# Kernel optimization log

Measured on AMD Instinct MI355X. Metric: run time of the kernel, lower is better.

The kernel has to match this reference:

```python
import jax, jax.numpy as jnp
import numpy as np

FILTERS = 256
B, H, W = 16, 64, 64
LN_EPS = 1e-5


def setup_inputs() -> dict:
    key = jax.random.key(0)
    ks = jax.random.split(key, 6)
    C = FILTERS
    scale = 1.0 / np.sqrt(C)  # kaiming-ish init for 1x1 convs
    return {
        "x": jax.random.normal(ks[0], (B, C, H, W), dtype=jnp.float32),
        "g": jax.random.normal(ks[1], (B, C, H, W), dtype=jnp.float32),
        "Wx": jax.random.normal(ks[2], (C, C), dtype=jnp.float32) * scale,
        "Wg": jax.random.normal(ks[3], (C, C), dtype=jnp.float32) * scale,
        "Wpsi": jax.random.normal(ks[4], (1, C), dtype=jnp.float32) * scale,
        "ln_gamma": jnp.ones((C,), dtype=jnp.float32),
        "ln_beta": jnp.zeros((C,), dtype=jnp.float32),
        "bxg": jnp.zeros((C,), dtype=jnp.float32),
        "bpsi": jnp.zeros((1,), dtype=jnp.float32),
    }


def reference(x, g, Wx, Wg, Wpsi, ln_gamma, ln_beta, bxg, bpsi):
    # 1x1 convs == per-pixel channel GEMMs: [B,C,H,W] x [O,C] -> [B,O,H,W]
    x_conv = jnp.einsum("bchw,oc->bohw", x, Wx)
    g_conv = jnp.einsum("bchw,oc->bohw", g, Wg)
    att = jax.nn.relu(x_conv + g_conv + bxg[None, :, None, None])
    # LayerNorm over channel dim (original permutes to NHWC, LN over last dim)
    mean = jnp.mean(att, axis=1, keepdims=True)
    var = jnp.mean(jnp.square(att - mean), axis=1, keepdims=True)
    att = (att - mean) * jax.lax.rsqrt(var + LN_EPS)
    att = att * ln_gamma[None, :, None, None] + ln_beta[None, :, None, None]
    # psi: 1x1 conv to single channel + bias, sigmoid gate
    att = jnp.einsum("bchw,oc->bohw", att, Wpsi) + bpsi[None, :, None, None]
    att = jax.nn.sigmoid(att)  # [B,1,H,W]
    return att * x
```

## Files before the change

kernel.cpp:

```cpp
#include <hip/hip_runtime.h>
#include <stdint.h>


typedef __bf16 bf16x8 __attribute__((ext_vector_type(8)));
typedef float f32x4 __attribute__((ext_vector_type(4)));

#define STR 40
#define LN_EPS 1e-5f

__device__ __forceinline__ uint16_t f2b(float f) {
    union { float f; uint32_t i; } v; v.f = f;
    uint32_t x = v.i;
    return (uint16_t)((x + 0x7FFFu + ((x >> 16) & 1u)) >> 16);
}

struct EpiShared {
    float red[3][4][256];
    float psi[256];
    float cpart[8];
};

union ALds {
    uint16_t a[2][2][256 * STR];
    EpiShared e;
};

__global__ void wconv_kernel(const float* __restrict__ Wx, const float* __restrict__ Wg,
                             uint16_t* __restrict__ ox, uint16_t* __restrict__ og) {
    const int i  = blockIdx.x * 256 + threadIdx.x;
    const int n  = i >> 6;
    const int k4 = (i & 63) * 4;
    const int it = k4 >> 5;
    const int kk = k4 & 31;
    const int dst = it * 8192 + n * 32 + kk;
    const float4 a = *(const float4*)&Wx[n * 256 + k4];
    const float4 b = *(const float4*)&Wg[n * 256 + k4];
    uint2 pa, pb;
    pa.x = (uint32_t)f2b(a.x) | ((uint32_t)f2b(a.y) << 16);
    pa.y = (uint32_t)f2b(a.z) | ((uint32_t)f2b(a.w) << 16);
    pb.x = (uint32_t)f2b(b.x) | ((uint32_t)f2b(b.y) << 16);
    pb.y = (uint32_t)f2b(b.z) | ((uint32_t)f2b(b.w) << 16);
    *(uint2*)&ox[dst] = pa;
    *(uint2*)&og[dst] = pb;
}

__device__ __forceinline__ void stage_load(float av[16], const float* __restrict__ Asrc,
                                           size_t abase, int c0, int px) {
    #pragma unroll
    for (int j = 0; j < 2; ++j)
        #pragma unroll
        for (int c = 0; c < 8; ++c)
            av[j * 8 + c] = Asrc[abase + (size_t)(c0 + j * 16 + c) * 4096 + px];
}

__device__ __forceinline__ void stage_store(const float av[16], uint16_t* dstrow, int c0) {
    #pragma unroll
    for (int j = 0; j < 2; ++j) {
        uint4 w;
        w.x = (uint32_t)f2b(av[j*8+0]) | ((uint32_t)f2b(av[j*8+1]) << 16);
        w.y = (uint32_t)f2b(av[j*8+2]) | ((uint32_t)f2b(av[j*8+3]) << 16);
        w.z = (uint32_t)f2b(av[j*8+4]) | ((uint32_t)f2b(av[j*8+5]) << 16);
        w.w = (uint32_t)f2b(av[j*8+6]) | ((uint32_t)f2b(av[j*8+7]) << 16);
        *(uint4*)&dstrow[c0 + j * 16] = w;
    }
}

__global__ __launch_bounds__(1024) void attgate_kernel(
    const float* __restrict__ x,
    const float* __restrict__ g,
    const uint16_t* __restrict__ Wxb,
    const uint16_t* __restrict__ Wgb,
    const float* __restrict__ Wpsi,
    const float* __restrict__ gamma,
    const float* __restrict__ beta,
    const float* __restrict__ bxg,
    const float* __restrict__ bpsi,
    float* __restrict__ out)
{
    __shared__ __align__(16) ALds u;

    const int t    = threadIdx.x;
    const int lane = t & 63;
    const int wv   = t >> 6;
    const int os   = wv & 3;
    const int ps   = wv >> 2;
    const int ln   = lane & 15;
    const int q    = lane >> 4;

    const int gp0  = blockIdx.x * 256;
    const int b    = gp0 >> 12;
    const int pix0 = gp0 & 4095;
    const size_t xbase = (size_t)b * (256 * 4096) + pix0;

    f32x4 acc[4][4];
    #pragma unroll
    for (int i = 0; i < 4; ++i)
        #pragma unroll
        for (int j = 0; j < 4; ++j)
            acc[i][j] = (f32x4){0.f, 0.f, 0.f, 0.f};

    const int at  = t & 511;
    const int px  = at & 255;
    const int cg  = at >> 8;
    const int c0  = cg * 8;
    const float* Asrc = (t < 512) ? x : g;
    const int tens    = (t < 512) ? 0 : 1;

    float av[16];
    stage_load(av, Asrc, xbase, c0, px);
    stage_store(av, &u.a[0][tens][px * STR], c0);

    const int fro = os * 64 + ln;

    for (int it = 0; it < 8; ++it) {
        __syncthreads();
        const int cur = it & 1;
        const uint16_t* Wxi = Wxb + it * 8192;
        const uint16_t* Wgi = Wgb + it * 8192;

        bf16x8 bx[4];
        #pragma unroll
        for (int nt = 0; nt < 4; ++nt)
            bx[nt] = *(const bf16x8*)&Wxi[(fro + nt * 16) * 32 + q * 8];

        if (it < 7)
            stage_load(av, Asrc, xbase + (size_t)((it + 1) * 32) * 4096, c0, px);

        bf16x8 af[4];
        #pragma unroll
        for (int mt = 0; mt < 4; ++mt)
            af[mt] = *(const bf16x8*)&u.a[cur][0][(ps * 64 + mt * 16 + ln) * STR + q * 8];
        #pragma unroll
        for (int mt = 0; mt < 4; ++mt)
            #pragma unroll
            for (int nt = 0; nt < 4; ++nt)
                acc[mt][nt] = __builtin_amdgcn_mfma_f32_16x16x32_bf16(af[mt], bx[nt], acc[mt][nt], 0, 0, 0);

        bf16x8 bg[4];
        #pragma unroll
        for (int nt = 0; nt < 4; ++nt)
            bg[nt] = *(const bf16x8*)&Wgi[(fro + nt * 16) * 32 + q * 8];
        #pragma unroll
        for (int mt = 0; mt < 4; ++mt)
            af[mt] = *(const bf16x8*)&u.a[cur][1][(ps * 64 + mt * 16 + ln) * STR + q * 8];
        #pragma unroll
        for (int mt = 0; mt < 4; ++mt)
            #pragma unroll
            for (int nt = 0; nt < 4; ++nt)
                acc[mt][nt] = __builtin_amdgcn_mfma_f32_16x16x32_bf16(af[mt], bg[nt], acc[mt][nt], 0, 0, 0);

        if (it < 7)
            stage_store(av, &u.a[cur ^ 1][tens][px * STR], c0);
    }

    __syncthreads();

    if (t < 256) {
        float a  = Wpsi[t] * gamma[t];
        float bb = Wpsi[t] * beta[t];
        #pragma unroll
        for (int off = 32; off; off >>= 1) {
            a  += __shfl_xor(a, off, 64);
            bb += __shfl_xor(bb, off, 64);
        }
        if (lane == 0) { u.e.cpart[wv] = a; u.e.cpart[4 + wv] = bb; }
    }

    float biasv[4], Ac[4];
    #pragma unroll
    for (int nt = 0; nt < 4; ++nt) {
        const int o = os * 64 + nt * 16 + ln;
        biasv[nt] = bxg[o];
        Ac[nt]    = Wpsi[o] * gamma[o];
    }
    __syncthreads();
    const float sumA = u.e.cpart[0] + u.e.cpart[1] + u.e.cpart[2] + u.e.cpart[3];
    const float sumB = u.e.cpart[4] + u.e.cpart[5] + u.e.cpart[6] + u.e.cpart[7];

    #pragma unroll
    for (int mt = 0; mt < 4; ++mt) {
        #pragma unroll
        for (int r = 0; r < 4; ++r) {
            float s = 0.f, ss = 0.f, tt = 0.f;
            #pragma unroll
            for (int nt = 0; nt < 4; ++nt) {
                float v = acc[mt][nt][r] + biasv[nt];
                v = fmaxf(v, 0.f);
                s += v; ss += v * v; tt += Ac[nt] * v;
            }
            #pragma unroll
            for (int off = 1; off < 16; off <<= 1) {
                s  += __shfl_xor(s,  off, 64);
                ss += __shfl_xor(ss, off, 64);
                tt += __shfl_xor(tt, off, 64);
            }
            if (ln == 0) {
                const int pix = ps * 64 + mt * 16 + q * 4 + r;
                u.e.red[0][os][pix] = s;
                u.e.red[1][os][pix] = ss;
                u.e.red[2][os][pix] = tt;
            }
        }
    }
    __syncthreads();

    if (t < 256) {
        const float s  = u.e.red[0][0][t] + u.e.red[0][1][t] + u.e.red[0][2][t] + u.e.red[0][3][t];
        const float ss = u.e.red[1][0][t] + u.e.red[1][1][t] + u.e.red[1][2][t] + u.e.red[1][3][t];
        const float tt = u.e.red[2][0][t] + u.e.red[2][1][t] + u.e.red[2][2][t] + u.e.red[2][3][t];
        const float mu   = s * (1.f / 256.f);
        const float var  = ss * (1.f / 256.f) - mu * mu;
        const float rstd = rsqrtf(var + LN_EPS);
        const float z    = rstd * (tt - mu * sumA) + sumB + bpsi[0];
        u.e.psi[t] = 1.f / (1.f + __expf(-z));
    }
    __syncthreads();

    const int pc = (t & 63) * 4;
    const float4 pv = *(const float4*)&u.e.psi[pc];
    const int crow = t >> 6;
    #pragma unroll
    for (int pass = 0; pass < 16; ++pass) {
        const int c = pass * 16 + crow;
        const size_t off = xbase + (size_t)c * 4096 + pc;
        const float4 d = *(const float4*)&x[off];
        float4 o;
        o.x = d.x * pv.x; o.y = d.y * pv.y; o.z = d.z * pv.z; o.w = d.w * pv.w;
        *(float4*)&out[off] = o;
    }
}

extern "C" void kernel_launch(void* const* d_in, const int* in_sizes, int n_in,
                              void* d_out, int out_size, void* d_ws, size_t ws_size,
                              hipStream_t stream) {
    const float* x    = (const float*)d_in[0];
    const float* g    = (const float*)d_in[1];
    const float* Wx   = (const float*)d_in[2];
    const float* Wg   = (const float*)d_in[3];
    const float* Wpsi = (const float*)d_in[4];
    const float* gam  = (const float*)d_in[5];
    const float* bet  = (const float*)d_in[6];
    const float* bxg  = (const float*)d_in[7];
    const float* bpsi = (const float*)d_in[8];
    float* out        = (float*)d_out;

    uint16_t* Wxb = (uint16_t*)d_ws;
    uint16_t* Wgb = (uint16_t*)((char*)d_ws + 131072);

    wconv_kernel<<<dim3(64), dim3(256), 0, stream>>>(Wx, Wg, Wxb, Wgb);
    attgate_kernel<<<dim3(256), dim3(1024), 0, stream>>>(
        x, g, Wxb, Wgb, Wpsi, gam, bet, bxg, bpsi, out);
}
```

Baseline: 213.0 us.

## Split gate multiply into separate kernel and shrink GEMM tiles to 64 pixels

Result: slower. 218.0 us (+2.3%).

```diff
diff --git a/kernel.cpp b/kernel.cpp
--- a/kernel.cpp
+++ b/kernel.cpp
@@ -15,13 +15,12 @@
 }
 
 struct EpiShared {
-    float red[3][4][256];
-    float psi[256];
+    float red[3][4][64];
     float cpart[8];
 };
 
 union ALds {
-    uint16_t a[2][2][256 * STR];
+    uint16_t a[2][2][64 * STR];
     EpiShared e;
 };
 
@@ -44,28 +43,23 @@
     *(uint2*)&og[dst] = pb;
 }
 
-__device__ __forceinline__ void stage_load(float av[16], const float* __restrict__ Asrc,
-                                           size_t abase, int c0, int px) {
-    #pragma unroll
-    for (int j = 0; j < 2; ++j)
-        #pragma unroll
-        for (int c = 0; c < 8; ++c)
-            av[j * 8 + c] = Asrc[abase + (size_t)(c0 + j * 16 + c) * 4096 + px];
-}
-
-__device__ __forceinline__ void stage_store(const float av[16], uint16_t* dstrow, int c0) {
-    #pragma unroll
-    for (int j = 0; j < 2; ++j) {
-        uint4 w;
-        w.x = (uint32_t)f2b(av[j*8+0]) | ((uint32_t)f2b(av[j*8+1]) << 16);
-        w.y = (uint32_t)f2b(av[j*8+2]) | ((uint32_t)f2b(av[j*8+3]) << 16);
-        w.z = (uint32_t)f2b(av[j*8+4]) | ((uint32_t)f2b(av[j*8+5]) << 16);
-        w.w = (uint32_t)f2b(av[j*8+6]) | ((uint32_t)f2b(av[j*8+7]) << 16);
-        *(uint4*)&dstrow[c0 + j * 16] = w;
-    }
-}
-
-__global__ __launch_bounds__(1024) void attgate_kernel(
+__device__ __forceinline__ void stage_load8(float av[8], const float* __restrict__ Asrc,
+                                            size_t abase, int c0, int px) {
+    #pragma unroll
+    for (int c = 0; c < 8; ++c)
+        av[c] = Asrc[abase + (size_t)(c0 + c) * 4096 + px];
+}
+
+__device__ __forceinline__ void stage_store8(const float av[8], uint16_t* dstrow, int c0) {
+    uint4 w;
+    w.x = (uint32_t)f2b(av[0]) | ((uint32_t)f2b(av[1]) << 16);
+    w.y = (uint32_t)f2b(av[2]) | ((uint32_t)f2b(av[3]) << 16);
+    w.z = (uint32_t)f2b(av[4]) | ((uint32_t)f2b(av[5]) << 16);
+    w.w = (uint32_t)f2b(av[6]) | ((uint32_t)f2b(av[7]) << 16);
+    *(uint4*)&dstrow[c0] = w;
+}
+
+__global__ __launch_bounds__(512, 6) void attgate_psi(
     const float* __restrict__ x,
     const float* __restrict__ g,
     const uint16_t* __restrict__ Wxb,
@@ -75,7 +69,7 @@
     const float* __restrict__ beta,
     const float* __restrict__ bxg,
     const float* __restrict__ bpsi,
-    float* __restrict__ out)
+    float* __restrict__ psi_g)
 {
     __shared__ __align__(16) ALds u;
 
@@ -87,28 +81,28 @@
     const int ln   = lane & 15;
     const int q    = lane >> 4;
 
-    const int gp0  = blockIdx.x * 256;
+    const int gp0  = blockIdx.x * 64;
     const int b    = gp0 >> 12;
     const int pix0 = gp0 & 4095;
     const size_t xbase = (size_t)b * (256 * 4096) + pix0;
 
-    f32x4 acc[4][4];
-    #pragma unroll
-    for (int i = 0; i < 4; ++i)
+    f32x4 acc[2][4];
+    #pragma unroll
+    for (int i = 0; i < 2; ++i)
         #pragma unroll
         for (int j = 0; j < 4; ++j)
             acc[i][j] = (f32x4){0.f, 0.f, 0.f, 0.f};
 
-    const int at  = t & 511;
-    const int px  = at & 255;
-    const int cg  = at >> 8;
+    const int at  = t & 255;
+    const int px  = at & 63;
+    const int cg  = at >> 6;
     const int c0  = cg * 8;
-    const float* Asrc = (t < 512) ? x : g;
-    const int tens    = (t < 512) ? 0 : 1;
-
-    float av[16];
-    stage_load(av, Asrc, xbase, c0, px);
-    stage_store(av, &u.a[0][tens][px * STR], c0);
+    const float* Asrc = (t < 256) ? x : g;
+    const int tens    = (t < 256) ? 0 : 1;
+
+    float av[8];
+    stage_load8(av, Asrc, xbase, c0, px);
+    stage_store8(av, &u.a[0][tens][px * STR], c0);
 
     const int fro = os * 64 + ln;
 
@@ -124,14 +118,14 @@
             bx[nt] = *(const bf16x8*)&Wxi[(fro + nt * 16) * 32 + q * 8];
 
         if (it < 7)
-            stage_load(av, Asrc, xbase + (size_t)((it + 1) * 32) * 4096, c0, px);
-
-        bf16x8 af[4];
-        #pragma unroll
-        for (int mt = 0; mt < 4; ++mt)
-            af[mt] = *(const bf16x8*)&u.a[cur][0][(ps * 64 + mt * 16 + ln) * STR + q * 8];
-        #pragma unroll
-        for (int mt = 0; mt < 4; ++mt)
+            stage_load8(av, Asrc, xbase + (size_t)((it + 1) * 32) * 4096, c0, px);
+
+        bf16x8 af[2];
+        #pragma unroll
+        for (int mt = 0; mt < 2; ++mt)
+            af[mt] = *(const bf16x8*)&u.a[cur][0][(ps * 32 + mt * 16 + ln) * STR + q * 8];
+        #pragma unroll
+        for (int mt = 0; mt < 2; ++mt)
             #pragma unroll
             for (int nt = 0; nt < 4; ++nt)
                 acc[mt][nt] = __builtin_amdgcn_mfma_f32_16x16x32_bf16(af[mt], bx[nt], acc[mt][nt], 0, 0, 0);
@@ -141,16 +135,16 @@
         for (int nt = 0; nt < 4; ++nt)
             bg[nt] = *(const bf16x8*)&Wgi[(fro + nt * 16) * 32 + q * 8];
         #pragma unroll
-        for (int mt = 0; mt < 4; ++mt)
-            af[mt] = *(const bf16x8*)&u.a[cur][1][(ps * 64 + mt * 16 + ln) * STR + q * 8];
-        #pragma unroll
-        for (int mt = 0; mt < 4; ++mt)
+        for (int mt = 0; mt < 2; ++mt)
+            af[mt] = *(const bf16x8*)&u.a[cur][1][(ps * 32 + mt * 16 + ln) * STR + q * 8];
+        #pragma unroll
+        for (int mt = 0; mt < 2; ++mt)
             #pragma unroll
             for (int nt = 0; nt < 4; ++nt)
                 acc[mt][nt] = __builtin_amdgcn_mfma_f32_16x16x32_bf16(af[mt], bg[nt], acc[mt][nt], 0, 0, 0);
 
         if (it < 7)
-            stage_store(av, &u.a[cur ^ 1][tens][px * STR], c0);
+            stage_store8(av, &u.a[cur ^ 1][tens][px * STR], c0);
     }
 
     __syncthreads();
@@ -178,7 +172,7 @@
     const float sumB = u.e.cpart[4] + u.e.cpart[5] + u.e.cpart[6] + u.e.cpart[7];
 
     #pragma unroll
-    for (int mt = 0; mt < 4; ++mt) {
+    for (int mt = 0; mt < 2; ++mt) {
         #pragma unroll
         for (int r = 0; r < 4; ++r) {
             float s = 0.f, ss = 0.f, tt = 0.f;
@@ -195,7 +189,7 @@
                 tt += __shfl_xor(tt, off, 64);
             }
             if (ln == 0) {
-                const int pix = ps * 64 + mt * 16 + q * 4 + r;
+                const int pix = ps * 32 + mt * 16 + q * 4 + r;
                 u.e.red[0][os][pix] = s;
                 u.e.red[1][os][pix] = ss;
                 u.e.red[2][os][pix] = tt;
@@ -204,7 +198,7 @@
     }
     __syncthreads();
 
-    if (t < 256) {
+    if (t < 64) {
         const float s  = u.e.red[0][0][t] + u.e.red[0][1][t] + u.e.red[0][2][t] + u.e.red[0][3][t];
         const float ss = u.e.red[1][0][t] + u.e.red[1][1][t] + u.e.red[1][2][t] + u.e.red[1][3][t];
         const float tt = u.e.red[2][0][t] + u.e.red[2][1][t] + u.e.red[2][2][t] + u.e.red[2][3][t];
@@ -212,21 +206,28 @@
         const float var  = ss * (1.f / 256.f) - mu * mu;
         const float rstd = rsqrtf(var + LN_EPS);
         const float z    = rstd * (tt - mu * sumA) + sumB + bpsi[0];
-        u.e.psi[t] = 1.f / (1.f + __expf(-z));
-    }
-    __syncthreads();
-
-    const int pc = (t & 63) * 4;
-    const float4 pv = *(const float4*)&u.e.psi[pc];
-    const int crow = t >> 6;
-    #pragma unroll
-    for (int pass = 0; pass < 16; ++pass) {
-        const int c = pass * 16 + crow;
-        const size_t off = xbase + (size_t)c * 4096 + pc;
-        const float4 d = *(const float4*)&x[off];
+        psi_g[gp0 + t] = 1.f / (1.f + __expf(-z));
+    }
+}
+
+__global__ __launch_bounds__(256) void gate_mul(
+    const float* __restrict__ x,
+    const float* __restrict__ psi,
+    float* __restrict__ out)
+{
+    const float4* __restrict__ x4  = (const float4*)x;
+    float4* __restrict__ o4        = (float4*)out;
+    int i = blockIdx.x * 256 + threadIdx.x;
+    #pragma unroll 1
+    for (; i < 4194304; i += 524288) {
+        const int b   = i >> 18;
+        const int rem = i & 262143;
+        const int p4  = rem & 1023;
+        const float4 pv = *(const float4*)&psi[(b << 12) + (p4 << 2)];
+        const float4 xv = x4[i];
         float4 o;
-        o.x = d.x * pv.x; o.y = d.y * pv.y; o.z = d.z * pv.z; o.w = d.w * pv.w;
-        *(float4*)&out[off] = o;
+        o.x = xv.x * pv.x; o.y = xv.y * pv.y; o.z = xv.z * pv.z; o.w = xv.w * pv.w;
+        o4[i] = o;
     }
 }
 
@@ -246,8 +247,10 @@
 
     uint16_t* Wxb = (uint16_t*)d_ws;
     uint16_t* Wgb = (uint16_t*)((char*)d_ws + 131072);
+    float*    psi = (float*)((char*)d_ws + 262144);
 
     wconv_kernel<<<dim3(64), dim3(256), 0, stream>>>(Wx, Wg, Wxb, Wgb);
-    attgate_kernel<<<dim3(256), dim3(1024), 0, stream>>>(
-        x, g, Wxb, Wgb, Wpsi, gam, bet, bxg, bpsi, out);
-}
+    attgate_psi<<<dim3(1024), dim3(512), 0, stream>>>(
+        x, g, Wxb, Wgb, Wpsi, gam, bet, bxg, bpsi, psi);
+    gate_mul<<<dim3(2048), dim3(256), 0, stream>>>(x, psi, out);
+}
```

## Vectorize activation staging loads to float4 and XOR-swizzle LDS tile

Applied to the files above, without the earlier changes.

Result: no change. 213.7 us (+0.3%).

```diff
diff --git a/kernel.cpp b/kernel.cpp
--- a/kernel.cpp
+++ b/kernel.cpp
@@ -13,6 +13,8 @@
     uint32_t x = v.i;
     return (uint16_t)((x + 0x7FFFu + ((x >> 16) & 1u)) >> 16);
 }
+
+__device__ __forceinline__ int swz(int px) { return ((px >> 3) & 3) << 4; }
 
 struct EpiShared {
     float red[3][4][256];
@@ -44,24 +46,24 @@
     *(uint2*)&og[dst] = pb;
 }
 
-__device__ __forceinline__ void stage_load(float av[16], const float* __restrict__ Asrc,
-                                           size_t abase, int c0, int px) {
-    #pragma unroll
-    for (int j = 0; j < 2; ++j)
-        #pragma unroll
-        for (int c = 0; c < 8; ++c)
-            av[j * 8 + c] = Asrc[abase + (size_t)(c0 + j * 16 + c) * 4096 + px];
-}
-
-__device__ __forceinline__ void stage_store(const float av[16], uint16_t* dstrow, int c0) {
-    #pragma unroll
-    for (int j = 0; j < 2; ++j) {
-        uint4 w;
-        w.x = (uint32_t)f2b(av[j*8+0]) | ((uint32_t)f2b(av[j*8+1]) << 16);
-        w.y = (uint32_t)f2b(av[j*8+2]) | ((uint32_t)f2b(av[j*8+3]) << 16);
-        w.z = (uint32_t)f2b(av[j*8+4]) | ((uint32_t)f2b(av[j*8+5]) << 16);
-        w.w = (uint32_t)f2b(av[j*8+6]) | ((uint32_t)f2b(av[j*8+7]) << 16);
-        *(uint4*)&dstrow[c0 + j * 16] = w;
+__device__ __forceinline__ void stage_load4(float4 av[4], const float* __restrict__ src,
+                                            size_t base, int ch0, int l) {
+    #pragma unroll
+    for (int j2 = 0; j2 < 4; ++j2)
+        av[j2] = *(const float4*)&src[base + (size_t)(ch0 + j2) * 4096 + 4 * l];
+}
+
+__device__ __forceinline__ void stage_store4(const float4 av[4], char* tile,
+                                             int w7, int l) {
+    const float* vf = (const float*)av;
+    #pragma unroll
+    for (int j = 0; j < 4; ++j) {
+        const int px = 4 * l + j;
+        uint2 d;
+        d.x = (uint32_t)f2b(vf[0 * 4 + j]) | ((uint32_t)f2b(vf[1 * 4 + j]) << 16);
+        d.y = (uint32_t)f2b(vf[2 * 4 + j]) | ((uint32_t)f2b(vf[3 * 4 + j]) << 16);
+        const int byte = (px * (STR * 2) + 8 * w7) ^ swz(px);
+        *(uint2*)(tile + byte) = d;
     }
 }
 
@@ -99,16 +101,14 @@
         for (int j = 0; j < 4; ++j)
             acc[i][j] = (f32x4){0.f, 0.f, 0.f, 0.f};
 
-    const int at  = t & 511;
-    const int px  = at & 255;
-    const int cg  = at >> 8;
-    const int c0  = cg * 8;
-    const float* Asrc = (t < 512) ? x : g;
-    const int tens    = (t < 512) ? 0 : 1;
-
-    float av[16];
-    stage_load(av, Asrc, xbase, c0, px);
-    stage_store(av, &u.a[0][tens][px * STR], c0);
+    const int w7   = wv & 7;
+    const int ch0  = 4 * w7;
+    const float* Asrc = (wv < 8) ? x : g;
+    const int tens    = (wv < 8) ? 0 : 1;
+
+    float4 av[4];
+    stage_load4(av, Asrc, xbase, ch0, lane);
+    stage_store4(av, (char*)&u.a[0][tens][0], w7, lane);
 
     const int fro = os * 64 + ln;
 
@@ -124,12 +124,15 @@
             bx[nt] = *(const bf16x8*)&Wxi[(fro + nt * 16) * 32 + q * 8];
 
         if (it < 7)
-            stage_load(av, Asrc, xbase + (size_t)((it + 1) * 32) * 4096, c0, px);
+            stage_load4(av, Asrc, xbase + (size_t)((it + 1) * 32) * 4096, ch0, lane);
 
         bf16x8 af[4];
         #pragma unroll
-        for (int mt = 0; mt < 4; ++mt)
-            af[mt] = *(const bf16x8*)&u.a[cur][0][(ps * 64 + mt * 16 + ln) * STR + q * 8];
+        for (int mt = 0; mt < 4; ++mt) {
+            const int px = ps * 64 + mt * 16 + ln;
+            af[mt] = *(const bf16x8*)((const char*)&u.a[cur][0][0] +
+                                      ((px * (STR * 2) + q * 16) ^ swz(px)));
+        }
         #pragma unroll
         for (int mt = 0; mt < 4; ++mt)
             #pragma unroll
@@ -141,8 +144,11 @@
         for (int nt = 0; nt < 4; ++nt)
             bg[nt] = *(const bf16x8*)&Wgi[(fro + nt * 16) * 32 + q * 8];
         #pragma unroll
-        for (int mt = 0; mt < 4; ++mt)
-            af[mt] = *(const bf16x8*)&u.a[cur][1][(ps * 64 + mt * 16 + ln) * STR + q * 8];
+        for (int mt = 0; mt < 4; ++mt) {
+            const int px = ps * 64 + mt * 16 + ln;
+            af[mt] = *(const bf16x8*)((const char*)&u.a[cur][1][0] +
+                                      ((px * (STR * 2) + q * 16) ^ swz(px)));
+        }
         #pragma unroll
         for (int mt = 0; mt < 4; ++mt)
             #pragma unroll
@@ -150,7 +156,7 @@
                 acc[mt][nt] = __builtin_amdgcn_mfma_f32_16x16x32_bf16(af[mt], bg[nt], acc[mt][nt], 0, 0, 0);
 
         if (it < 7)
-            stage_store(av, &u.a[cur ^ 1][tens][px * STR], c0);
+            stage_store4(av, (char*)&u.a[cur ^ 1][tens][0], w7, lane);
     }
 
     __syncthreads();
```
